# Performance work log

Measured on AMD Instinct MI355X. Metric: run time of the kernel, lower is better.

## Reference

```python
import jax, jax.numpy as jnp
import numpy as np

C = 64          # channels
K = 15          # sum(shell_sizes)=1+14
H = 32          # neighbors per query
N = 50000       # support points (== query points M)
RADIUS = 1.0
SIGMA = 0.7
INF = 1e6
BN_EPS = 1e-5


def _init_kernel_points(key):
    # stand-in for load_kernels: 1 center point + 14 points on a sphere shell
    pts = jax.random.normal(key, (K - 1, 3), dtype=jnp.float32)
    pts = pts / jnp.linalg.norm(pts, axis=1, keepdims=True) * RADIUS
    return jnp.concatenate([jnp.zeros((1, 3), jnp.float32), pts], axis=0)


def setup_inputs() -> dict:
    key = jax.random.key(0)
    ks = jax.random.split(key, 10)
    q_pts = jax.random.normal(ks[0], (N, 3), dtype=jnp.float32)
    s_pts = jax.random.normal(ks[1], (N, 3), dtype=jnp.float32)
    s_feats = jax.random.normal(ks[2], (N, C), dtype=jnp.float32)
    neighb_inds = jax.random.randint(ks[3], (N, H), 0, N)
    kernel_points = _init_kernel_points(ks[4])
    # alpha_mlp: Linear(C->C, no bias) -> BatchNorm -> LeakyReLU(0.1) -> Linear(C->K*C)
    lim1 = 1.0 / np.sqrt(C)
    W1 = jax.random.uniform(ks[5], (C, C), jnp.float32, -lim1, lim1)
    gamma = jnp.ones((C,), jnp.float32)
    beta = jnp.zeros((C,), jnp.float32)
    W2 = jax.random.uniform(ks[6], (C, K * C), jnp.float32, -lim1, lim1)
    b2 = jax.random.uniform(ks[7], (K * C,), jnp.float32, -lim1, lim1)
    return {"q_pts": q_pts, "s_pts": s_pts, "s_feats": s_feats,
            "neighb_inds": neighb_inds, "kernel_points": kernel_points,
            "W1": W1, "gamma": gamma, "beta": beta, "W2": W2, "b2": b2}


def reference(q_pts, s_pts, s_feats, neighb_inds, kernel_points, W1, gamma, beta, W2, b2):
    M = q_pts.shape[0]
    # alpha_mlp on pooled (= center) features: (M, C) -> (M, K*C)
    h = s_feats @ W1
    mu = jnp.mean(h, axis=0)
    var = jnp.var(h, axis=0)
    h = (h - mu) / jnp.sqrt(var + BN_EPS) * gamma + beta
    h = jax.nn.leaky_relu(h, 0.1)
    conv_weights = (h @ W2 + b2).reshape(M, K, C)

    # gather neighbor features with a zero padding row (index N -> zeros)
    padded_feats = jnp.concatenate([s_feats, jnp.zeros((1, C), s_feats.dtype)], axis=0)
    neighbor_feats = padded_feats[neighb_inds]                 # (M, H, C)

    # relative neighbor positions with inf padding point
    s_pts_pad = jnp.concatenate([s_pts, jnp.full((1, 3), INF, s_pts.dtype)], axis=0)
    neighbors = s_pts_pad[neighb_inds] - q_pts[:, None, :]     # (M, H, 3)

    # kernel-point influence: nearest kernel point + linear influence
    diff = neighbors[:, :, None, :] - kernel_points            # (M, H, K, 3)
    sq_d = jnp.sum(diff * diff, axis=-1)                       # (M, H, K)
    nn_sq = jnp.min(sq_d, axis=-1)                             # (M, H)
    nn_idx = jnp.argmin(sq_d, axis=-1)                         # (M, H)
    infl = jnp.clip(1.0 - jnp.sqrt(nn_sq) / SIGMA, 0.0)        # (M, H)

    # per-neighbor channel weights from the MLP output, gathered by 1nn kernel point
    nw = jnp.take_along_axis(conv_weights, nn_idx[:, :, None], axis=1)  # (M, H, C)
    nw = nw * infl[:, :, None]

    # weighted aggregation (merge=mul, aggr=sum over neighbors)
    return jnp.sum(neighbor_feats * nw, axis=1)                # (M, C)
```

## Files before the change

### kernel.cpp

```cpp
#include <hip/hip_runtime.h>
#include <math.h>

#define N_PTS 50000
#define CCH   64
#define KP    15
#define NH    32
#define SIGMA 0.7f
#define BN_EPS 1e-5f
#define LEAKY 0.1f
#define QB    16
#define NTILES 60
#define CWS   18

typedef short bf16x8 __attribute__((ext_vector_type(8)));
typedef float floatx4 __attribute__((ext_vector_type(4)));

__device__ __forceinline__ unsigned short f2b(float f) {
    union { float f; unsigned u; } v; v.f = f;
    return (unsigned short)((v.u + 0x7FFFu + ((v.u >> 16) & 1u)) >> 16);
}
__device__ __forceinline__ float b2f(unsigned short b) {
    union { unsigned u; float f; } v; v.u = ((unsigned)b) << 16;
    return v.f;
}

__global__ void k_w2prep(const float* __restrict__ W2, unsigned short* __restrict__ w2b) {
    int g = blockIdx.x * 256 + threadIdx.x;
    int lane = g & 63, s = (g >> 6) & 1, tt = g >> 7;
    int col = lane & 15, quad = lane >> 4;
    ushort4 lo, hi;
    int base = (s * 32 + quad * 8) * 960 + tt * 16 + col;
    lo.x = f2b(W2[base + 0 * 960]); lo.y = f2b(W2[base + 1 * 960]);
    lo.z = f2b(W2[base + 2 * 960]); lo.w = f2b(W2[base + 3 * 960]);
    hi.x = f2b(W2[base + 4 * 960]); hi.y = f2b(W2[base + 5 * 960]);
    hi.z = f2b(W2[base + 6 * 960]); hi.w = f2b(W2[base + 7 * 960]);
    *(ushort4*)(w2b + g * 8)     = lo;
    *(ushort4*)(w2b + g * 8 + 4) = hi;
}

__global__ __launch_bounds__(256) void k_bn_stats(const float* __restrict__ sf,
                                                  const float* __restrict__ W1,
                                                  float* __restrict__ bn) {
    int t = threadIdx.x;
    int c = t & 63, ml = t >> 6;
    float w1c[64];
    #pragma unroll
    for (int i = 0; i < 64; ++i) w1c[i] = W1[i * 64 + c];
    __shared__ float rows[4][64];
    float acc_s = 0.f, acc_q = 0.f;
    int stride = gridDim.x * 4;
    for (int m0 = blockIdx.x * 4; m0 < N_PTS; m0 += stride) {
        __syncthreads();
        ((float*)rows)[t] = sf[m0 * 64 + t];
        __syncthreads();
        float h = 0.f;
        #pragma unroll
        for (int i4 = 0; i4 < 16; ++i4) {
            float4 r = *(const float4*)&rows[ml][i4 * 4];
            h += r.x * w1c[i4 * 4] + r.y * w1c[i4 * 4 + 1]
               + r.z * w1c[i4 * 4 + 2] + r.w * w1c[i4 * 4 + 3];
        }
        acc_s += h;
        acc_q += h * h;
    }
    __shared__ float red[2][256];
    red[0][t] = acc_s; red[1][t] = acc_q;
    __syncthreads();
    if (t < 64) {
        float s = red[0][t] + red[0][64 + t] + red[0][128 + t] + red[0][192 + t];
        float q = red[1][t] + red[1][64 + t] + red[1][128 + t] + red[1][192 + t];
        atomicAdd(&bn[t], s);
        atomicAdd(&bn[64 + t], q);
    }
}

__global__ void k_bn_final(const float* __restrict__ bn,
                           const float* __restrict__ gamma,
                           const float* __restrict__ beta,
                           float* __restrict__ ab) {
    int c = threadIdx.x;
    if (c < 64) {
        float mu  = bn[c] * (1.0f / N_PTS);
        float var = bn[64 + c] * (1.0f / N_PTS) - mu * mu;
        float a   = gamma[c] * rsqrtf(var + BN_EPS);
        ab[c]      = a;
        ab[64 + c] = beta[c] - mu * a;
    }
}

__global__ __launch_bounds__(256, 3) void k_main(
    const float* __restrict__ q_pts, const float* __restrict__ s_pts,
    const float* __restrict__ s_feats, const int* __restrict__ nb,
    const float* __restrict__ kpts, const float* __restrict__ W1,
    const float* __restrict__ b2, const unsigned short* __restrict__ w2b,
    const float* __restrict__ ab, float* __restrict__ out) {

    __shared__ __align__(16) unsigned short Afrag[2][64][8];
    __shared__ __align__(16) unsigned short cwT[960 * CWS];
    __shared__ float rows16[QB][64];
    __shared__ float kp[KP * 3];
    __shared__ int   nCnt[QB];
    __shared__ int   nIdxL[QB][NH];
    __shared__ float nInfL[QB][NH];
    __shared__ int   nKL[QB][NH];

    int t = threadIdx.x;
    int m0 = blockIdx.x * QB;
    int lane = t & 63;
    int wv = t >> 6;

    if (t < KP * 3) kp[t] = kpts[t];
    if (t >= 240) nCnt[t - 240] = 0;
    {
        int q = t >> 4, i4 = t & 15;
        *(float4*)&rows16[q][i4 * 4] = *(const float4*)&s_feats[(m0 + q) * 64 + i4 * 4];
    }
    __syncthreads();

    {
        int c = lane;
        float w1c[64];
        #pragma unroll
        for (int i = 0; i < 64; ++i) w1c[i] = W1[i * 64 + c];
        float a = ab[c], bs = ab[64 + c];
        int s = c >> 5, quad = (c >> 3) & 3, j = c & 7;
        #pragma unroll
        for (int jj = 0; jj < 4; ++jj) {
            int q = wv * 4 + jj;
            float h = 0.f;
            #pragma unroll
            for (int i4 = 0; i4 < 16; ++i4) {
                float4 r = *(const float4*)&rows16[q][i4 * 4];
                h += r.x * w1c[i4 * 4] + r.y * w1c[i4 * 4 + 1]
                   + r.z * w1c[i4 * 4 + 2] + r.w * w1c[i4 * 4 + 3];
            }
            h = a * h + bs;
            h = h > 0.f ? h : LEAKY * h;
            Afrag[s][quad * 16 + q][j] = f2b(h);
        }
    }
    __syncthreads();

    {
        bf16x8 a0 = *(const bf16x8*)&Afrag[0][lane][0];
        bf16x8 a1 = *(const bf16x8*)&Afrag[1][lane][0];
        int col = lane & 15, quad = lane >> 4;
        for (int ti = 0; ti < 15; ++ti) {
            int tt = wv * 15 + ti;
            bf16x8 bf0 = *(const bf16x8*)(w2b + ((tt * 2 + 0) * 64 + lane) * 8);
            bf16x8 bf1 = *(const bf16x8*)(w2b + ((tt * 2 + 1) * 64 + lane) * 8);
            floatx4 acc = {0.f, 0.f, 0.f, 0.f};
            acc = __builtin_amdgcn_mfma_f32_16x16x32_bf16(a0, bf0, acc, 0, 0, 0);
            acc = __builtin_amdgcn_mfma_f32_16x16x32_bf16(a1, bf1, acc, 0, 0, 0);
            int n = tt * 16 + col;
            float bb = b2[n];
            unsigned short* dst = &cwT[n * CWS + quad * 4];
            ushort2 w01, w23;
            w01.x = f2b(acc[0] + bb); w01.y = f2b(acc[1] + bb);
            w23.x = f2b(acc[2] + bb); w23.y = f2b(acc[3] + bb);
            *(ushort2*)(dst)     = w01;
            *(ushort2*)(dst + 2) = w23;
        }
    }

    for (int task = t; task < QB * NH; task += 256) {
        int q = task >> 5, hh = task & 31;
        int m = m0 + q;
        int idx = nb[m * NH + hh];
        float px = s_pts[idx * 3 + 0] - q_pts[m * 3 + 0];
        float py = s_pts[idx * 3 + 1] - q_pts[m * 3 + 1];
        float pz = s_pts[idx * 3 + 2] - q_pts[m * 3 + 2];
        float best = 1e30f; int bi = 0;
        #pragma unroll
        for (int k = 0; k < KP; ++k) {
            float dx = px - kp[k * 3], dy = py - kp[k * 3 + 1], dz = pz - kp[k * 3 + 2];
            float d = dx * dx + dy * dy + dz * dz;
            if (d < best) { best = d; bi = k; }
        }
        float infl = 1.f - sqrtf(best) * (1.0f / SIGMA);
        if (infl > 0.f) {
            int pos = atomicAdd(&nCnt[q], 1);
            nIdxL[q][pos] = idx;
            nInfL[q][pos] = infl;
            nKL[q][pos]   = bi;
        }
    }
    __syncthreads();

    {
        int c = lane;
        #pragma unroll
        for (int qi = 0; qi < 4; ++qi) {
            int q = wv * 4 + qi;
            int na = nCnt[q];
            float acc = 0.f;
            for (int jj = 0; jj < na; ++jj) {
                int   idx  = nIdxL[q][jj];
                float infl = nInfL[q][jj];
                int   k    = nKL[q][jj];
                float f = s_feats[idx * 64 + c];
                float w = b2f(cwT[(k * 64 + c) * CWS + q]);
                acc += infl * f * w;
            }
            out[(m0 + q) * 64 + c] = acc;
        }
    }
}

extern "C" void kernel_launch(void* const* d_in, const int* in_sizes, int n_in,
                              void* d_out, int out_size, void* d_ws, size_t ws_size,
                              hipStream_t stream) {
    const float* q_pts   = (const float*)d_in[0];
    const float* s_pts   = (const float*)d_in[1];
    const float* s_feats = (const float*)d_in[2];
    const int*   nb      = (const int*)d_in[3];
    const float* kpts    = (const float*)d_in[4];
    const float* W1      = (const float*)d_in[5];
    const float* gamma   = (const float*)d_in[6];
    const float* beta    = (const float*)d_in[7];
    const float* W2      = (const float*)d_in[8];
    const float* b2      = (const float*)d_in[9];
    float* out = (float*)d_out;

    float* ws = (float*)d_ws;
    float* bn = ws;
    float* ab = ws + 128;
    unsigned short* w2b = (unsigned short*)(ws + 256);

    hipMemsetAsync(bn, 0, 128 * sizeof(float), stream);
    k_w2prep<<<30, 256, 0, stream>>>(W2, w2b);
    k_bn_stats<<<1024, 256, 0, stream>>>(s_feats, W1, bn);
    k_bn_final<<<1, 64, 0, stream>>>(bn, gamma, beta, ab);
    k_main<<<N_PTS / QB, 256, 0, stream>>>(q_pts, s_pts, s_feats, nb, kpts,
                                           W1, b2, w2b, ab, out);
}
```

Before: 186.2 us.

## Cache first-layer MLP output in bf16 and fold BN finalize into main kernel

The stats kernel now also stores the pre-BN hidden activations h in bf16 to workspace, and the W2 conversion is merged into the same launch, leaving two launches where there were four. The main kernel recomputes the BN scale/shift per block from the raw sums, loads h directly into MFMA A fragments instead of redoing the W1 matmul, packs neighbor index and kernel id into one int, and unrolls the aggregation loop by two. Occupancy hint raised from 3 to 4. It trades extra global writes and reads of h, plus bf16 rounding of h before BN, for removing the per-block W1 recompute and the launch overhead.

Measured after the change: 161.8 us. 1.15x faster.

```diff
diff --git a/kernel.cpp b/kernel.cpp
--- a/kernel.cpp
+++ b/kernel.cpp
@@ -9,8 +9,8 @@
 #define BN_EPS 1e-5f
 #define LEAKY 0.1f
 #define QB    16
-#define NTILES 60
 #define CWS   18
+#define STATS_BLOCKS 512
 
 typedef short bf16x8 __attribute__((ext_vector_type(8)));
 typedef float floatx4 __attribute__((ext_vector_type(4)));
@@ -24,32 +24,34 @@
     return v.f;
 }
 
-__global__ void k_w2prep(const float* __restrict__ W2, unsigned short* __restrict__ w2b) {
-    int g = blockIdx.x * 256 + threadIdx.x;
-    int lane = g & 63, s = (g >> 6) & 1, tt = g >> 7;
-    int col = lane & 15, quad = lane >> 4;
-    ushort4 lo, hi;
-    int base = (s * 32 + quad * 8) * 960 + tt * 16 + col;
-    lo.x = f2b(W2[base + 0 * 960]); lo.y = f2b(W2[base + 1 * 960]);
-    lo.z = f2b(W2[base + 2 * 960]); lo.w = f2b(W2[base + 3 * 960]);
-    hi.x = f2b(W2[base + 4 * 960]); hi.y = f2b(W2[base + 5 * 960]);
-    hi.z = f2b(W2[base + 6 * 960]); hi.w = f2b(W2[base + 7 * 960]);
-    *(ushort4*)(w2b + g * 8)     = lo;
-    *(ushort4*)(w2b + g * 8 + 4) = hi;
-}
-
-__global__ __launch_bounds__(256) void k_bn_stats(const float* __restrict__ sf,
-                                                  const float* __restrict__ W1,
-                                                  float* __restrict__ bn) {
+__global__ __launch_bounds__(256) void k_prep(const float* __restrict__ sf,
+                                              const float* __restrict__ W1,
+                                              const float* __restrict__ W2,
+                                              float* __restrict__ bn,
+                                              unsigned short* __restrict__ hst,
+                                              unsigned short* __restrict__ w2b) {
     int t = threadIdx.x;
+    if (blockIdx.x >= STATS_BLOCKS) {
+        int g = (blockIdx.x - STATS_BLOCKS) * 256 + t;
+        int lane = g & 63, s = (g >> 6) & 1, tt = g >> 7;
+        int col = lane & 15, quad = lane >> 4;
+        int base = (s * 32 + quad * 8) * 960 + tt * 16 + col;
+        ushort4 lo, hi;
+        lo.x = f2b(W2[base + 0 * 960]); lo.y = f2b(W2[base + 1 * 960]);
+        lo.z = f2b(W2[base + 2 * 960]); lo.w = f2b(W2[base + 3 * 960]);
+        hi.x = f2b(W2[base + 4 * 960]); hi.y = f2b(W2[base + 5 * 960]);
+        hi.z = f2b(W2[base + 6 * 960]); hi.w = f2b(W2[base + 7 * 960]);
+        *(ushort4*)(w2b + g * 8)     = lo;
+        *(ushort4*)(w2b + g * 8 + 4) = hi;
+        return;
+    }
     int c = t & 63, ml = t >> 6;
     float w1c[64];
     #pragma unroll
     for (int i = 0; i < 64; ++i) w1c[i] = W1[i * 64 + c];
     __shared__ float rows[4][64];
     float acc_s = 0.f, acc_q = 0.f;
-    int stride = gridDim.x * 4;
-    for (int m0 = blockIdx.x * 4; m0 < N_PTS; m0 += stride) {
+    for (int m0 = blockIdx.x * 4; m0 < N_PTS; m0 += STATS_BLOCKS * 4) {
         __syncthreads();
         ((float*)rows)[t] = sf[m0 * 64 + t];
         __syncthreads();
@@ -62,6 +64,7 @@
         }
         acc_s += h;
         acc_q += h * h;
+        hst[(m0 + ml) * 64 + c] = f2b(h);
     }
     __shared__ float red[2][256];
     red[0][t] = acc_s; red[1][t] = acc_q;
@@ -74,76 +77,56 @@
     }
 }
 
-__global__ void k_bn_final(const float* __restrict__ bn,
-                           const float* __restrict__ gamma,
-                           const float* __restrict__ beta,
-                           float* __restrict__ ab) {
-    int c = threadIdx.x;
-    if (c < 64) {
-        float mu  = bn[c] * (1.0f / N_PTS);
-        float var = bn[64 + c] * (1.0f / N_PTS) - mu * mu;
-        float a   = gamma[c] * rsqrtf(var + BN_EPS);
-        ab[c]      = a;
-        ab[64 + c] = beta[c] - mu * a;
-    }
-}
-
-__global__ __launch_bounds__(256, 3) void k_main(
+__global__ __launch_bounds__(256, 4) void k_main(
     const float* __restrict__ q_pts, const float* __restrict__ s_pts,
     const float* __restrict__ s_feats, const int* __restrict__ nb,
-    const float* __restrict__ kpts, const float* __restrict__ W1,
+    const float* __restrict__ kpts, const float* __restrict__ gamma,
+    const float* __restrict__ beta, const float* __restrict__ bn,
     const float* __restrict__ b2, const unsigned short* __restrict__ w2b,
-    const float* __restrict__ ab, float* __restrict__ out) {
-
-    __shared__ __align__(16) unsigned short Afrag[2][64][8];
+    const unsigned short* __restrict__ hst, float* __restrict__ out) {
+
     __shared__ __align__(16) unsigned short cwT[960 * CWS];
-    __shared__ float rows16[QB][64];
-    __shared__ float kp[KP * 3];
+    __shared__ float abS[128];
+    __shared__ float kp[48];
     __shared__ int   nCnt[QB];
-    __shared__ int   nIdxL[QB][NH];
-    __shared__ float nInfL[QB][NH];
-    __shared__ int   nKL[QB][NH];
+    __shared__ int   nPack[QB][NH];
+    __shared__ float nInf[QB][NH];
 
     int t = threadIdx.x;
+    int lane = t & 63, wv = t >> 6;
     int m0 = blockIdx.x * QB;
-    int lane = t & 63;
-    int wv = t >> 6;
-
+
+    if (t < 64) {
+        float mu  = bn[t] * (1.0f / N_PTS);
+        float var = bn[64 + t] * (1.0f / N_PTS) - mu * mu;
+        float a   = gamma[t] * rsqrtf(var + BN_EPS);
+        abS[t]      = a;
+        abS[64 + t] = beta[t] - mu * a;
+    }
     if (t < KP * 3) kp[t] = kpts[t];
     if (t >= 240) nCnt[t - 240] = 0;
+    __syncthreads();
+
+    int row = lane & 15, half = lane >> 4;
+    bf16x8 a0, a1;
     {
-        int q = t >> 4, i4 = t & 15;
-        *(float4*)&rows16[q][i4 * 4] = *(const float4*)&s_feats[(m0 + q) * 64 + i4 * 4];
-    }
-    __syncthreads();
+        const unsigned short* hrow = hst + (m0 + row) * 64 + half * 8;
+        bf16x8 r0 = *(const bf16x8*)(hrow);
+        bf16x8 r1 = *(const bf16x8*)(hrow + 32);
+        #pragma unroll
+        for (int j = 0; j < 8; ++j) {
+            int c0 = half * 8 + j;
+            float g0 = abS[c0] * b2f((unsigned short)r0[j]) + abS[64 + c0];
+            g0 = g0 > 0.f ? g0 : LEAKY * g0;
+            a0[j] = (short)f2b(g0);
+            int c1 = 32 + half * 8 + j;
+            float g1 = abS[c1] * b2f((unsigned short)r1[j]) + abS[64 + c1];
+            g1 = g1 > 0.f ? g1 : LEAKY * g1;
+            a1[j] = (short)f2b(g1);
+        }
+    }
 
     {
-        int c = lane;
-        float w1c[64];
-        #pragma unroll
-        for (int i = 0; i < 64; ++i) w1c[i] = W1[i * 64 + c];
-        float a = ab[c], bs = ab[64 + c];
-        int s = c >> 5, quad = (c >> 3) & 3, j = c & 7;
-        #pragma unroll
-        for (int jj = 0; jj < 4; ++jj) {
-            int q = wv * 4 + jj;
-            float h = 0.f;
-            #pragma unroll
-            for (int i4 = 0; i4 < 16; ++i4) {
-                float4 r = *(const float4*)&rows16[q][i4 * 4];
-                h += r.x * w1c[i4 * 4] + r.y * w1c[i4 * 4 + 1]
-                   + r.z * w1c[i4 * 4 + 2] + r.w * w1c[i4 * 4 + 3];
-            }
-            h = a * h + bs;
-            h = h > 0.f ? h : LEAKY * h;
-            Afrag[s][quad * 16 + q][j] = f2b(h);
-        }
-    }
-    __syncthreads();
-
-    {
-        bf16x8 a0 = *(const bf16x8*)&Afrag[0][lane][0];
-        bf16x8 a1 = *(const bf16x8*)&Afrag[1][lane][0];
         int col = lane & 15, quad = lane >> 4;
         for (int ti = 0; ti < 15; ++ti) {
             int tt = wv * 15 + ti;
@@ -180,9 +163,8 @@
         float infl = 1.f - sqrtf(best) * (1.0f / SIGMA);
         if (infl > 0.f) {
             int pos = atomicAdd(&nCnt[q], 1);
-            nIdxL[q][pos] = idx;
-            nInfL[q][pos] = infl;
-            nKL[q][pos]   = bi;
+            nPack[q][pos] = idx | (bi << 20);
+            nInf[q][pos]  = infl;
         }
     }
     __syncthreads();
@@ -194,13 +176,21 @@
             int q = wv * 4 + qi;
             int na = nCnt[q];
             float acc = 0.f;
-            for (int jj = 0; jj < na; ++jj) {
-                int   idx  = nIdxL[q][jj];
-                float infl = nInfL[q][jj];
-                int   k    = nKL[q][jj];
-                float f = s_feats[idx * 64 + c];
-                float w = b2f(cwT[(k * 64 + c) * CWS + q]);
-                acc += infl * f * w;
+            int jj = 0;
+            for (; jj + 1 < na; jj += 2) {
+                int p0 = nPack[q][jj], p1 = nPack[q][jj + 1];
+                float i0 = nInf[q][jj], i1 = nInf[q][jj + 1];
+                float f0 = s_feats[(p0 & 0xFFFFF) * 64 + c];
+                float f1 = s_feats[(p1 & 0xFFFFF) * 64 + c];
+                float w0 = b2f(cwT[((p0 >> 20) * 64 + c) * CWS + q]);
+                float w1 = b2f(cwT[((p1 >> 20) * 64 + c) * CWS + q]);
+                acc += i0 * f0 * w0 + i1 * f1 * w1;
+            }
+            if (jj < na) {
+                int p0 = nPack[q][jj];
+                float f0 = s_feats[(p0 & 0xFFFFF) * 64 + c];
+                float w0 = b2f(cwT[((p0 >> 20) * 64 + c) * CWS + q]);
+                acc += nInf[q][jj] * f0 * w0;
             }
             out[(m0 + q) * 64 + c] = acc;
         }
@@ -224,13 +214,11 @@
 
     float* ws = (float*)d_ws;
     float* bn = ws;
-    float* ab = ws + 128;
-    unsigned short* w2b = (unsigned short*)(ws + 256);
+    unsigned short* w2b = (unsigned short*)(ws + 128);
+    unsigned short* hst = w2b + 61440;
 
     hipMemsetAsync(bn, 0, 128 * sizeof(float), stream);
-    k_w2prep<<<30, 256, 0, stream>>>(W2, w2b);
-    k_bn_stats<<<1024, 256, 0, stream>>>(s_feats, W1, bn);
-    k_bn_final<<<1, 64, 0, stream>>>(bn, gamma, beta, ab);
+    k_prep<<<STATS_BLOCKS + 30, 256, 0, stream>>>(s_feats, W1, W2, bn, hst, w2b);
     k_main<<<N_PTS / QB, 256, 0, stream>>>(q_pts, s_pts, s_feats, nb, kpts,
-                                           W1, b2, w2b, ab, out);
-}
+                                           gamma, beta, bn, b2, w2b, hst, out);
+}
```
